# Kernel optimization log

Hardware: AMD Instinct MI355X
Metric: run time of the kernel (lower is better)

## Reference

```python
import jax, jax.numpy as jnp
import numpy as np

B = 2048
N_PATCH = 196  # 14x14 grid of 2x2 patches over 28x28

CNOT = jnp.array([[1, 0, 0, 0],
                  [0, 1, 0, 0],
                  [0, 0, 0, 1],
                  [0, 0, 1, 0]], dtype=jnp.complex64)


def ry_mat(t):
    c = jnp.cos(t / 2).astype(jnp.complex64)
    s = jnp.sin(t / 2).astype(jnp.complex64)
    return jnp.stack([jnp.stack([c, -s], -1), jnp.stack([s, c], -1)], -2)


def rx_mat(t):
    c = jnp.cos(t / 2).astype(jnp.complex64)
    s = (-1j) * jnp.sin(t / 2).astype(jnp.complex64)
    return jnp.stack([jnp.stack([c, s], -1), jnp.stack([s, c], -1)], -2)


def _apply_1q(state, mat, wire):
    # state: [B, P, 2,2,2,2]; mat: [2,2] or [B,P,2,2]
    s = jnp.moveaxis(state, 2 + wire, -1)
    shp = s.shape
    s = s.reshape(shp[0], shp[1], -1, 2)
    if mat.ndim == 2:
        s = jnp.einsum('ij,bpkj->bpki', mat, s)
    else:
        s = jnp.einsum('bpij,bpkj->bpki', mat, s)
    return jnp.moveaxis(s.reshape(shp), -1, 2 + wire)


def _apply_2q(state, mat, w0, w1):
    s = jnp.moveaxis(state, (2 + w0, 2 + w1), (-2, -1))
    shp = s.shape
    s = s.reshape(shp[0], shp[1], -1, 4)  # last dim = (w0,w1) combined
    s = jnp.einsum('ij,bpkj->bpki', mat, s)
    return jnp.moveaxis(s.reshape(shp), (-2, -1), (2 + w0, 2 + w1))


def setup_inputs() -> dict:
    key = jax.random.key(0)
    k1, k2, k3 = jax.random.split(key, 3)
    x = jax.random.normal(k1, (B, 784), dtype=jnp.float32)
    q_params = jax.random.normal(k2, (4,), dtype=jnp.float32)
    W = jax.random.normal(k3, (10, 784), dtype=jnp.float32) * 0.02
    b = jnp.zeros((10,), dtype=jnp.float32)
    return {'x': x, 'q_params': q_params, 'W': W, 'b': b}


def reference(x, q_params, W, b):
    Bsz = x.shape[0]
    # extract all 2x2 stride-2 patches at once: [B,196,4] ordered
    # (x[r,c], x[r,c+1], x[r+1,c], x[r+1,c+1]) matching the torch loop
    patches = x.reshape(Bsz, 14, 2, 14, 2).transpose(0, 1, 3, 2, 4).reshape(Bsz, N_PATCH, 4)
    # init |0000> state for every (batch, patch)
    state = jnp.zeros((Bsz, N_PATCH, 2, 2, 2, 2), dtype=jnp.complex64)
    state = state.at[:, :, 0, 0, 0, 0].set(1.0)
    # encoder: RY(pixel) on each wire
    for w in range(4):
        state = _apply_1q(state, ry_mat(patches[:, :, w]), w)
    # fixed 8-op random layer (shared params across all patches)
    state = _apply_1q(state, ry_mat(q_params[0]), 0)
    state = _apply_1q(state, rx_mat(q_params[1]), 1)
    state = _apply_2q(state, CNOT, 0, 1)
    state = _apply_1q(state, ry_mat(q_params[2]), 2)
    state = _apply_2q(state, CNOT, 1, 2)
    state = _apply_1q(state, rx_mat(q_params[3]), 3)
    state = _apply_2q(state, CNOT, 2, 3)
    state = _apply_2q(state, CNOT, 3, 0)
    # PauliZ expectation per wire: sum_k |amp_k|^2 * (1 - 2*bit_w(k))
    probs = jnp.abs(state.reshape(Bsz, N_PATCH, 16)) ** 2
    bits = (jnp.arange(16)[:, None] >> jnp.arange(3, -1, -1)[None, :]) & 1
    signs = (1 - 2 * bits).astype(jnp.float32)  # [16, 4]
    meas = jnp.einsum('bpk,kw->bpw', probs, signs)  # [B,196,4]
    features = meas.reshape(Bsz, 784)
    logits = features @ W.T + b
    return jax.nn.log_softmax(logits, axis=-1)
```

## Files before the change

### kernel.cpp

```cpp
#include <hip/hip_runtime.h>


constexpr int NPIX = 784;
constexpr int NP   = 196;
constexpr int NCLS = 10;

template <int Ctrl, int RowMask>
__device__ __forceinline__ float dpp_add(float x) {
    int s = __builtin_amdgcn_update_dpp(0, __float_as_int(x), Ctrl, RowMask, 0xf, false);
    return x + __int_as_float(s);
}

__global__ __launch_bounds__(256)
void quanv_fused(const float* __restrict__ x,
                 const float* __restrict__ qp,
                 const float* __restrict__ W,
                 const float* __restrict__ bias,
                 float* __restrict__ out)
{
    const int b   = blockIdx.x;
    const int tid = threadIdx.x;

    const float t0 = qp[0];
    const float c1 = __cosf(qp[1]);
    const float t2 = qp[2];
    const float c3 = __cosf(qp[3]);

    float part[NCLS];
#pragma unroll
    for (int j = 0; j < NCLS; ++j) part[j] = 0.f;

    if (tid < NP) {
        const int pr = tid / 14;
        const int pc = tid - pr * 14;
        const float* xrow = x + b * NPIX + (2 * pr) * 28 + 2 * pc;
        const float2 top = *reinterpret_cast<const float2*>(xrow);
        const float2 bot = *reinterpret_cast<const float2*>(xrow + 28);

        const float z0 = __cosf(top.x + t0);
        const float z1 = __cosf(top.y) * c1;
        const float z2 = __cosf(bot.x + t2);
        const float z3 = __cosf(bot.y) * c3;

        const float f1 = z0 * z1;
        const float f2 = f1 * z2;
        const float f3 = f2 * z3;
        const float f0 = z1 * z2 * z3;

        const float4* Wp = reinterpret_cast<const float4*>(W) + tid;
#pragma unroll
        for (int j = 0; j < NCLS; ++j) {
            const float4 w = Wp[j * (NPIX / 4)];
            part[j] = fmaf(f0, w.x, fmaf(f1, w.y, fmaf(f2, w.z, f3 * w.w)));
        }
    }

#pragma unroll
    for (int j = 0; j < NCLS; ++j) {
        float v = part[j];
        v = dpp_add<0x111, 0xf>(v);
        v = dpp_add<0x112, 0xf>(v);
        v = dpp_add<0x114, 0xf>(v);
        v = dpp_add<0x118, 0xf>(v);
        v = dpp_add<0x142, 0xa>(v);
        v = dpp_add<0x143, 0xc>(v);
        part[j] = v;
    }

    __shared__ float sred[4][NCLS];
    const int wave = tid >> 6;
    const int lane = tid & 63;
    if (lane == 63) {
#pragma unroll
        for (int j = 0; j < NCLS; ++j) sred[wave][j] = part[j];
    }
    __syncthreads();

    if (tid == 0) {
        float logit[NCLS];
        float m = -1e30f;
#pragma unroll
        for (int j = 0; j < NCLS; ++j) {
            logit[j] = sred[0][j] + sred[1][j] + sred[2][j] + sred[3][j] + bias[j];
            m = fmaxf(m, logit[j]);
        }
        float s = 0.f;
#pragma unroll
        for (int j = 0; j < NCLS; ++j) s += __expf(logit[j] - m);
        const float lse = m + __logf(s);
        float2* o2 = reinterpret_cast<float2*>(out + b * NCLS);
#pragma unroll
        for (int j = 0; j < NCLS / 2; ++j)
            o2[j] = make_float2(logit[2 * j] - lse, logit[2 * j + 1] - lse);
    }
}

extern "C" void kernel_launch(void* const* d_in, const int* in_sizes, int n_in,
                              void* d_out, int out_size, void* d_ws, size_t ws_size,
                              hipStream_t stream) {
    const float* x    = (const float*)d_in[0];
    const float* qp   = (const float*)d_in[1];
    const float* W    = (const float*)d_in[2];
    const float* bias = (const float*)d_in[3];
    float* out = (float*)d_out;

    const int B = in_sizes[0] / NPIX;
    quanv_fused<<<B, 256, 0, stream>>>(x, qp, W, bias, out);
}
```

Baseline: 10.29 us.

## Map one batch row per wavefront and drop the LDS cross-wave reduction

Each 64-lane wave now processes a whole batch sample, with each lane looping over up to four patches, so a block covers four samples. This removes the shared-memory staging, the __syncthreads barrier and the single-thread finalisation, and it makes use of the 60 lanes that previously sat idle in the fourth wave. The cost is that each lane does four times the work serially, including four times as many W loads, and the grid shrinks to a quarter of its former size, which lowers parallelism.

```diff
diff --git a/kernel.cpp b/kernel.cpp
--- a/kernel.cpp
+++ b/kernel.cpp
@@ -12,46 +12,57 @@
 }
 
 __global__ __launch_bounds__(256)
-void quanv_fused(const float* __restrict__ x,
-                 const float* __restrict__ qp,
-                 const float* __restrict__ W,
-                 const float* __restrict__ bias,
-                 float* __restrict__ out)
+void quanv_wave(const float* __restrict__ x,
+                const float* __restrict__ qp,
+                const float* __restrict__ W,
+                const float* __restrict__ bias,
+                float* __restrict__ out,
+                int B)
 {
-    const int b   = blockIdx.x;
-    const int tid = threadIdx.x;
+    const int tid  = threadIdx.x;
+    const int wave = tid >> 6;
+    const int lane = tid & 63;
+    const int b    = blockIdx.x * 4 + wave;
+    if (b >= B) return;
 
     const float t0 = qp[0];
     const float c1 = __cosf(qp[1]);
     const float t2 = qp[2];
     const float c3 = __cosf(qp[3]);
 
+    const float* __restrict__ xb = x + b * NPIX;
+
     float part[NCLS];
 #pragma unroll
     for (int j = 0; j < NCLS; ++j) part[j] = 0.f;
 
-    if (tid < NP) {
-        const int pr = tid / 14;
-        const int pc = tid - pr * 14;
-        const float* xrow = x + b * NPIX + (2 * pr) * 28 + 2 * pc;
-        const float2 top = *reinterpret_cast<const float2*>(xrow);
-        const float2 bot = *reinterpret_cast<const float2*>(xrow + 28);
+#pragma unroll
+    for (int i = 0; i < 4; ++i) {
+        const int p = lane + 64 * i;
+        if (i < 3 || lane < NP - 192) {
+            const unsigned pu = (unsigned)p;
+            const int pr = (int)((pu * 4682u) >> 16);
+            const int pc = p - pr * 14;
+            const float* xr = xb + pr * 56 + pc * 2;
+            const float2 top = *reinterpret_cast<const float2*>(xr);
+            const float2 bot = *reinterpret_cast<const float2*>(xr + 28);
 
-        const float z0 = __cosf(top.x + t0);
-        const float z1 = __cosf(top.y) * c1;
-        const float z2 = __cosf(bot.x + t2);
-        const float z3 = __cosf(bot.y) * c3;
+            const float z0 = __cosf(top.x + t0);
+            const float z1 = __cosf(top.y) * c1;
+            const float z2 = __cosf(bot.x + t2);
+            const float z3 = __cosf(bot.y) * c3;
 
-        const float f1 = z0 * z1;
-        const float f2 = f1 * z2;
-        const float f3 = f2 * z3;
-        const float f0 = z1 * z2 * z3;
+            const float f1 = z0 * z1;
+            const float f2 = f1 * z2;
+            const float f3 = f2 * z3;
+            const float f0 = z1 * z2 * z3;
 
-        const float4* Wp = reinterpret_cast<const float4*>(W) + tid;
+            const float4* Wp = reinterpret_cast<const float4*>(W) + p;
 #pragma unroll
-        for (int j = 0; j < NCLS; ++j) {
-            const float4 w = Wp[j * (NPIX / 4)];
-            part[j] = fmaf(f0, w.x, fmaf(f1, w.y, fmaf(f2, w.z, f3 * w.w)));
+            for (int j = 0; j < NCLS; ++j) {
+                const float4 w = Wp[j * (NPIX / 4)];
+                part[j] += fmaf(f0, w.x, fmaf(f1, w.y, fmaf(f2, w.z, f3 * w.w)));
+            }
         }
     }
 
@@ -67,21 +78,12 @@
         part[j] = v;
     }
 
-    __shared__ float sred[4][NCLS];
-    const int wave = tid >> 6;
-    const int lane = tid & 63;
     if (lane == 63) {
-#pragma unroll
-        for (int j = 0; j < NCLS; ++j) sred[wave][j] = part[j];
-    }
-    __syncthreads();
-
-    if (tid == 0) {
         float logit[NCLS];
         float m = -1e30f;
 #pragma unroll
         for (int j = 0; j < NCLS; ++j) {
-            logit[j] = sred[0][j] + sred[1][j] + sred[2][j] + sred[3][j] + bias[j];
+            logit[j] = part[j] + bias[j];
             m = fmaxf(m, logit[j]);
         }
         float s = 0.f;
@@ -105,5 +107,6 @@
     float* out = (float*)d_out;
 
     const int B = in_sizes[0] / NPIX;
-    quanv_fused<<<B, 256, 0, stream>>>(x, qp, W, bias, out);
+    const int grid = (B + 3) / 4;
+    quanv_wave<<<grid, 256, 0, stream>>>(x, qp, W, bias, out, B);
 }
```

After: 10.25 us. Within noise of the previous version (-0.4%).
